# Optimization experiments

Measured on AMD Instinct MI355X. Metric: run time of the kernel, lower is better.

The kernel has to match this reference:

```python
import jax, jax.numpy as jnp
import numpy as np

PS = 3        # patch_size
RATE = 2      # rate
FS = 3        # fuse_kernel_size
SS = 10.0     # softmax_scale
PAD = (PS - 1) // 2       # tl.calc_padding(ps, 1)
FUSE_PAD = (FS - 1) // 2  # tl.calc_padding(fs, 1)
EPS = 1e-4


def extract_patches(x, ps, stride, pad):
    """x: (B,C,H,W) -> (B, L, C, ps, ps); L row-major over output positions (== F.unfold order)."""
    B, C, H, W = x.shape
    xp = jnp.pad(x, ((0, 0), (0, 0), (pad, pad), (pad, pad)))
    oh = (H + 2 * pad - ps) // stride + 1
    ow = (W + 2 * pad - ps) // stride + 1
    rows = []
    for dy in range(ps):  # small fixed loop (ps=3)
        cols = []
        for dx in range(ps):
            cols.append(xp[:, :, dy:dy + (oh - 1) * stride + 1:stride,
                              dx:dx + (ow - 1) * stride + 1:stride])
        rows.append(jnp.stack(cols, axis=2))           # (B,C,ps,oh,ow)
    p = jnp.stack(rows, axis=2)                        # (B,C,ps,ps,oh,ow)
    return p.reshape(B, C, ps, ps, oh * ow).transpose(0, 4, 1, 2, 3)


def diag_fuse(S, fs, pad):
    """conv2d of (N,N) 'image' with identity fs x fs kernel (diagonal smoothing)."""
    N = S.shape[0]
    Sp = jnp.pad(S, ((pad, pad), (pad, pad)))
    out = Sp[0:N, 0:N]
    for k in range(1, fs):  # fs=3, tiny fixed loop
        out = out + Sp[k:k + N, k:k + N]
    return out


def fuse_scores(S, hr, wr):
    L = hr * wr
    S = diag_fuse(S, FS, FUSE_PAD)
    S = S.reshape(hr, wr, hr, wr).transpose(1, 0, 3, 2).reshape(L, L)
    S = diag_fuse(S, FS, FUSE_PAD)
    S = S.reshape(wr, hr, wr, hr).transpose(1, 0, 3, 2).reshape(L, L)
    return S


def contextual_attention(f_o, b_o, mask_o):
    B, c, h, w = f_o.shape
    # nearest downsample by 1/rate == strided slice
    f = f_o[:, :, ::RATE, ::RATE]
    b = b_o[:, :, ::RATE, ::RATE]
    m = mask_o[:, :, ::RATE, ::RATE]
    hr, wr = f.shape[2], f.shape[3]
    L = hr * wr

    fg = extract_patches(f, PS, 1, PAD)        # (B,L,c,ps,ps) foreground neighborhoods
    bs = extract_patches(b, PS, 1, PAD)        # (B,L,c,ps,ps) shrunk bg patches
    bi = extract_patches(b_o, PS, RATE, PAD)   # (B,L,c,ps,ps) full-res bg patches

    bnorm = jnp.maximum(jnp.sqrt(jnp.sum(bs * bs, axis=(2, 3, 4))), EPS)  # (B,L)
    bsn = bs / bnorm[:, :, None, None, None]

    # score[b,p,q] = <normalized bg patch p, fg neighborhood at position q>
    S = jnp.einsum('bpcij,bqcij->bpq', bsn, fg)  # (B,L,L)
    S = jax.vmap(lambda s: fuse_scores(s, hr, wr))(S)

    # valid-patch indicator from downsampled mask
    mp = extract_patches(m, PS, 1, PAD)                                   # (B,L,1,ps,ps)
    valid = (jnp.mean(mp, axis=(2, 3, 4)) == 0.0).astype(f_o.dtype)       # (B,L)

    score = S.reshape(B, L, hr, wr) * valid[:, :, None, None]
    score = jax.nn.softmax(score * SS, axis=1) * valid[:, :, None, None]

    # conv_transpose2d(score, bi, stride=RATE, padding=PAD, output_padding=1) / 4
    wgt = jnp.flip(bi.transpose(0, 2, 1, 3, 4), axis=(-2, -1))  # (B,c,L,ps,ps)
    pad_cfg = [(PS - 1 - PAD, PS - 1 - PAD + 1)] * 2            # output_padding on high side

    def agg(s, wk):  # s:(L,hr,wr), wk:(c,L,ps,ps)
        return jax.lax.conv_general_dilated(
            s[None], wk, (1, 1), pad_cfg, lhs_dilation=(RATE, RATE),
            dimension_numbers=('NCHW', 'OIHW', 'NCHW'))[0]

    out = jax.vmap(agg)(score, wgt) / 4.0   # (B,c,h,w)
    return out


def setup_inputs() -> dict:
    key = jax.random.key(0)
    k1, k2, k3 = jax.random.split(key, 3)
    f_o = jax.random.normal(k1, (16, 128, 64, 64), dtype=jnp.float32)
    b_o = jax.random.normal(k2, (16, 128, 64, 64), dtype=jnp.float32)
    mask_o = jax.random.randint(k3, (16, 1, 64, 64), 0, 2).astype(jnp.float32)
    return {"f_o": f_o, "b_o": b_o, "mask_o": mask_o}


def reference(f_o, b_o, mask_o):
    return contextual_attention(f_o, b_o, mask_o)
```

## Files before the change

### kernel.cpp

```cpp
#include <hip/hip_runtime.h>
#include <cmath>

#define CC 128
#define HH 64
#define WWI 64
#define LL 1024
#define NB 16
#define MM 1152
#define KC 384
#define TPD 1156

#define SLAB      2977808ul
#define OFF_TP    0
#define OFF_S3T   0
#define OFF_W     0
#define OFF_S2    1336336
#define OFF_SCORET 1336336
#define OFF_POOL  2384912
#define OFF_N2    2974736
#define OFF_BNORM 2975760
#define OFF_VALID 2976784

typedef __bf16 bf16x8 __attribute__((ext_vector_type(8)));
typedef __bf16 bf16x4 __attribute__((ext_vector_type(4)));
typedef float f32x4 __attribute__((ext_vector_type(4)));

#define GLDS(g, l) __builtin_amdgcn_global_load_lds( \
    (const __attribute__((address_space(1))) unsigned int*)(const void*)(g), \
    (__attribute__((address_space(3))) unsigned int*)(void*)(l), 16, 0, 0)

__global__ __launch_bounds__(256) void k_prep(const float* __restrict__ f_o,
                                              const float* __restrict__ b_o,
                                              float* __restrict__ ws,
                                              int b0) {
    int bz = blockIdx.y, gb = b0 + bz;
    int uy = blockIdx.x;
    __shared__ float lf[128 * 33];
    __shared__ float lb[128 * 33];
    __shared__ float red[8 * 32];
    int tid = threadIdx.x;
    int ux = tid & 31, co = tid >> 5;
    size_t pix = (size_t)(2 * uy) * WWI + 2 * ux;
    const float* fbp = f_o + (size_t)gb * CC * HH * WWI + pix;
    const float* bbp = b_o + (size_t)gb * CC * HH * WWI + pix;
#pragma unroll
    for (int pass = 0; pass < 16; pass++) {
        int c = pass * 8 + co;
        lf[c * 33 + ux] = fbp[(size_t)c * HH * WWI];
        lb[c * 33 + ux] = bbp[(size_t)c * HH * WWI];
    }
    __syncthreads();
    int ux2 = tid >> 3, cg = (tid & 7) * 16;
    int u = uy * 32 + ux2;
    __bf16* bcat = (__bf16*)(ws + (size_t)bz * SLAB + OFF_POOL) + (size_t)u * KC;
    __bf16* fcat = bcat + 393216;
    float s2 = 0.f;
#pragma unroll
    for (int k = 0; k < 16; k++) {
        int c = cg + k;
        float fv = lf[c * 33 + ux2];
        float bv = lb[c * 33 + ux2];
        __bf16 fhi = (__bf16)fv; __bf16 flo = (__bf16)(fv - (float)fhi);
        __bf16 bhi = (__bf16)bv; __bf16 blo = (__bf16)(bv - (float)bhi);
        bcat[c] = bhi; bcat[128 + c] = bhi; bcat[256 + c] = blo;
        fcat[c] = fhi; fcat[128 + c] = flo; fcat[256 + c] = fhi;
        s2 += bv * bv;
    }
    red[(tid & 7) * 32 + ux2] = s2;
    __syncthreads();
    if (tid < 32) {
        float s = 0.f;
#pragma unroll
        for (int k = 0; k < 8; k++) s += red[k * 32 + tid];
        ws[(size_t)bz * SLAB + OFF_N2 + uy * 32 + tid] = s;
    }
}

__global__ __launch_bounds__(256) void k_bnorm_valid(float* __restrict__ ws,
                                                     const float* __restrict__ mask,
                                                     int b0) {
    int t = blockIdx.x * 256 + threadIdx.x;
    int p  = t & (LL - 1);
    int bz = t >> 10;
    int gb = b0 + bz;
    int py = p >> 5, px = p & 31;
    const float* mb = mask + (size_t)gb * HH * WWI;
    const float* n2 = ws + (size_t)bz * SLAB + OFF_N2;
    float s = 0.f, msum = 0.f;
#pragma unroll
    for (int dy = -1; dy <= 1; dy++) {
#pragma unroll
        for (int dx = -1; dx <= 1; dx++) {
            int py2 = py + dy, px2 = px + dx;
            if ((unsigned)py2 < 32u && (unsigned)px2 < 32u) {
                s    += n2[(py2 << 5) | px2];
                msum += mb[(2 * py2) * WWI + 2 * px2];
            }
        }
    }
    ws[(size_t)bz * SLAB + OFF_BNORM + p] = fmaxf(sqrtf(s), 1e-4f);
    ws[(size_t)bz * SLAB + OFF_VALID + p] = (msum == 0.0f) ? 1.0f : 0.0f;
}

__global__ __launch_bounds__(256) void k_zerohalo(float* __restrict__ ws) {
    int bz = blockIdx.y;
    int R  = blockIdx.x;
    float* Tr = ws + (size_t)bz * SLAB + OFF_TP + (size_t)R * TPD;
    int a = R / 34, b = R - 34 * a;
    bool rowhalo = (a == 0) | (a == 33) | (b == 0) | (b == 33);
    for (int c = threadIdx.x; c < TPD; c += 256) {
        int cy = c / 34, cb = c - 34 * cy;
        if (rowhalo | (cy == 0) | (cy == 33) | (cb == 0) | (cb == 33))
            Tr[c] = 0.f;
    }
}

template<int KTOT>
__device__ __forceinline__ void gemm_core(const __bf16* __restrict__ Ab,
                                          const __bf16* __restrict__ Bb,
                                          int lda, int ldb, int m0, int n0,
                                          __bf16* As, __bf16* Bs,
                                          f32x4 acc[4][4]) {
    int t = threadIdx.x;
    int lane = t & 63, w = t >> 6;
    int rsub = lane >> 3;
    int g8   = ((lane & 7) ^ (rsub & 7)) * 8;
    int lm = lane & 15, kgf = lane >> 4;
    int wm = (w & 1) * 64, wn = (w >> 1) * 64;

    for (int k0 = 0; k0 < KTOT; k0 += 64) {
        __syncthreads();
#pragma unroll
        for (int ci = 0; ci < 4; ci++) {
            int rb = ci * 32 + w * 8;
            int r  = rb + rsub;
            GLDS(Ab + (size_t)(m0 + r) * lda + k0 + g8, &As[rb * 64]);
            GLDS(Bb + (size_t)(n0 + r) * ldb + k0 + g8, &Bs[rb * 64]);
        }
        __syncthreads();
#pragma unroll
        for (int s2 = 0; s2 < 2; s2++) {
            bf16x8 af[4], bfr[4];
#pragma unroll
            for (int i = 0; i < 4; i++)
                af[i] = *(const bf16x8*)&As[(wm + i * 16 + lm) * 64 + (((s2 * 4 + kgf) ^ (lm & 7)) * 8)];
#pragma unroll
            for (int j = 0; j < 4; j++)
                bfr[j] = *(const bf16x8*)&Bs[(wn + j * 16 + lm) * 64 + (((s2 * 4 + kgf) ^ (lm & 7)) * 8)];
#pragma unroll
            for (int i = 0; i < 4; i++)
#pragma unroll
                for (int j = 0; j < 4; j++)
                    acc[i][j] = __builtin_amdgcn_mfma_f32_16x16x32_bf16(af[i], bfr[j], acc[i][j], 0, 0, 0);
        }
    }
}

__global__ __launch_bounds__(256) void k_gemm_T_mfma(float* __restrict__ ws) {
    int bz = blockIdx.z;
    const __bf16* Ab = (const __bf16*)(ws + (size_t)bz * SLAB + OFF_POOL);
    const __bf16* Bb = Ab + 393216;
    float* Tp = ws + (size_t)bz * SLAB + OFF_TP;
    int m0 = blockIdx.y * 128, n0 = blockIdx.x * 128;
    __shared__ __align__(16) __bf16 As[128 * 64];
    __shared__ __align__(16) __bf16 Bs[128 * 64];
    f32x4 acc[4][4];
#pragma unroll
    for (int i = 0; i < 4; i++)
#pragma unroll
        for (int j = 0; j < 4; j++) acc[i][j] = (f32x4)0.0f;
    gemm_core<KC>(Ab, Bb, KC, KC, m0, n0, As, Bs, acc);
    int lane = threadIdx.x & 63, w = threadIdx.x >> 6;
    int lm = lane & 15, kgf = lane >> 4;
    int wm = (w & 1) * 64, wn = (w >> 1) * 64;
#pragma unroll
    for (int i = 0; i < 4; i++) {
#pragma unroll
        for (int r = 0; r < 4; r++) {
            int m = m0 + wm + i * 16 + kgf * 4 + r;
            float* dst = Tp + (size_t)(((m >> 5) + 1) * 34 + (m & 31) + 1) * TPD;
#pragma unroll
            for (int j = 0; j < 4; j++) {
                int v = n0 + wn + j * 16 + lm;
                dst[((v >> 5) + 1) * 34 + (v & 31) + 1] = acc[i][j][r];
            }
        }
    }
}

__global__ __launch_bounds__(256) void k_s12(float* __restrict__ ws) {
    int bz = blockIdx.y;
    int i0 = blockIdx.x * 8;
    const float* Tp = ws + (size_t)bz * SLAB + OFF_TP;
    const float* bn = ws + (size_t)bz * SLAB + OFF_BNORM;
    float* S2 = ws + (size_t)bz * SLAB + OFF_S2;
    __shared__ float Dsh[10][1024];
    int tid = threadIdx.x;
    for (int rl = 0; rl < 10; rl++) {
        int r = i0 - 1 + rl;
        if ((unsigned)r >= 1024u) continue;
        float invr = 1.0f / bn[r];
        size_t rbase = (size_t)(((r >> 5) + 1) * 34 + (r & 31) + 1) * TPD;
#pragma unroll
        for (int so = 0; so < 4; so++) {
            int s = so * 256 + tid;
            const float* cb = Tp + rbase + ((s >> 5) + 1) * 34 + (s & 31) + 1;
            float d = 0.f;
#pragma unroll
            for (int dy = -1; dy <= 1; dy++)
#pragma unroll
                for (int dx = -1; dx <= 1; dx++)
                    d += cb[dy * (34 * TPD + 34) + dx * (TPD + 1)];
            Dsh[rl][s] = d * invr;
        }
    }
    __syncthreads();
#pragma unroll
    for (int il = 0; il < 8; il++) {
        int i = i0 + il;
        float* orow = S2 + (size_t)i * LL;
#pragma unroll
        for (int jo = 0; jo < 4; jo++) {
            int j = jo * 256 + tid;
            float acc = 0.f;
#pragma unroll
            for (int k1 = -1; k1 <= 1; k1++) {
                int r = i + k1, s = j + k1;
                if ((unsigned)r < 1024u && (unsigned)s < 1024u)
                    acc += Dsh[il + 1 + k1][s];
            }
            orow[j] = acc;
        }
    }
}

__global__ __launch_bounds__(256) void k_st3t(float* __restrict__ ws) {
    int bz = blockIdx.z;
    const float* ib = ws + (size_t)bz * SLAB + OFF_S2;
    float* ob = ws + (size_t)bz * SLAB + OFF_S3T;
    int p0 = blockIdx.y * 64, q0 = blockIdx.x * 64;
    __shared__ float tile[64][65];
    int t = threadIdx.x;
#pragma unroll
    for (int it = 0; it < 16; it++) {
        int e = it * 256 + t;
        int pl = e >> 6, ql = e & 63;
        int p = p0 + pl, q = q0 + ql;
        int sp = ((p & 31) << 5) | (p >> 5);
        int sq = ((q & 31) << 5) | (q >> 5);
        float acc = 0.f;
#pragma unroll
        for (int k = -1; k <= 1; k++) {
            int tp = sp + k, tq = sq + k;
            if ((unsigned)tp < 1024u && (unsigned)tq < 1024u) {
                int row = ((tp & 31) << 5) | (tp >> 5);
                int col = ((tq & 31) << 5) | (tq >> 5);
                acc += ib[(size_t)row * LL + col];
            }
        }
        tile[pl][ql] = acc;
    }
    __syncthreads();
#pragma unroll
    for (int it = 0; it < 16; it++) {
        int e = it * 256 + t;
        int ql = e >> 6, pl = e & 63;
        ob[(size_t)(q0 + ql) * LL + p0 + pl] = tile[pl][ql];
    }
}

__global__ __launch_bounds__(256) void k_softmax_bf(float* __restrict__ ws) {
    int bz = blockIdx.z;
    int lane = threadIdx.x & 63;
    int q = blockIdx.x * 4 + (threadIdx.x >> 6);
    const float* row = ws + (size_t)bz * SLAB + OFF_S3T + (size_t)q * LL;
    const float* vb  = ws + (size_t)bz * SLAB + OFF_VALID;
    __bf16* orow = (__bf16*)(ws + (size_t)bz * SLAB + OFF_SCORET) + (size_t)q * LL;

    float4 v[4], vl[4];
#pragma unroll
    for (int i = 0; i < 4; i++) {
        int p = lane * 4 + i * 256;
        float4 s = *(const float4*)(row + p);
        float4 m = *(const float4*)(vb + p);
        v[i] = {s.x * m.x, s.y * m.y, s.z * m.z, s.w * m.w};
        vl[i] = m;
    }
    float mx = -1e30f;
#pragma unroll
    for (int i = 0; i < 4; i++)
        mx = fmaxf(mx, fmaxf(fmaxf(v[i].x, v[i].y), fmaxf(v[i].z, v[i].w)));
#pragma unroll
    for (int k = 1; k < 64; k <<= 1)
        mx = fmaxf(mx, __shfl_xor(mx, k, 64));
    float sum = 0.f;
    float4 e[4];
#pragma unroll
    for (int i = 0; i < 4; i++) {
        e[i].x = __expf(10.f * (v[i].x - mx));
        e[i].y = __expf(10.f * (v[i].y - mx));
        e[i].z = __expf(10.f * (v[i].z - mx));
        e[i].w = __expf(10.f * (v[i].w - mx));
        sum += e[i].x + e[i].y + e[i].z + e[i].w;
    }
#pragma unroll
    for (int k = 1; k < 64; k <<= 1)
        sum += __shfl_xor(sum, k, 64);
    float inv = 1.0f / sum;
#pragma unroll
    for (int i = 0; i < 4; i++) {
        bf16x4 o;
        o[0] = (__bf16)(e[i].x * inv * vl[i].x);
        o[1] = (__bf16)(e[i].y * inv * vl[i].y);
        o[2] = (__bf16)(e[i].z * inv * vl[i].z);
        o[3] = (__bf16)(e[i].w * inv * vl[i].w);
        *(bf16x4*)(orow + lane * 4 + i * 256) = o;
    }
}

__global__ __launch_bounds__(256) void k_makeA(const float* __restrict__ b_o,
                                               float* __restrict__ ws,
                                               int b0) {
    int bz = blockIdx.z, gb = b0 + bz;
    int e = blockIdx.x * 256 + threadIdx.x;
    int m = e >> 10, p = e & 1023;
    int c = m / 9, rem = m - 9 * c, jy = rem / 3, jx = rem - 3 * jy;
    int row = 2 * (p >> 5) + jy - 1;
    int col = 2 * (p & 31) + jx - 1;
    float v = 0.f;
    if ((unsigned)row < 64u && (unsigned)col < 64u)
        v = b_o[((size_t)(gb * CC + c) * HH + row) * WWI + col];
    ((__bf16*)(ws + (size_t)bz * SLAB + OFF_POOL))[(size_t)m * LL + p] = (__bf16)v;
}

__global__ __launch_bounds__(256) void k_gemm_W_mfma(float* __restrict__ ws) {
    int bz = blockIdx.z;
    const __bf16* Ab = (const __bf16*)(ws + (size_t)bz * SLAB + OFF_POOL);
    const __bf16* Bb = (const __bf16*)(ws + (size_t)bz * SLAB + OFF_SCORET);
    float* Wb = ws + (size_t)bz * SLAB + OFF_W;
    int m0 = blockIdx.y * 128, n0 = blockIdx.x * 128;
    __shared__ __align__(16) __bf16 As[128 * 64];
    __shared__ __align__(16) __bf16 Bs[128 * 64];
    f32x4 acc[4][4];
#pragma unroll
    for (int i = 0; i < 4; i++)
#pragma unroll
        for (int j = 0; j < 4; j++) acc[i][j] = (f32x4)0.0f;
    gemm_core<LL>(Ab, Bb, LL, LL, m0, n0, As, Bs, acc);
    int lane = threadIdx.x & 63, w = threadIdx.x >> 6;
    int lm = lane & 15, kgf = lane >> 4;
    int wm = (w & 1) * 64, wn = (w >> 1) * 64;
#pragma unroll
    for (int i = 0; i < 4; i++) {
#pragma unroll
        for (int r = 0; r < 4; r++) {
            int m = m0 + wm + i * 16 + kgf * 4 + r;
            float* dst = Wb + (size_t)m * LL + n0 + wn + lm;
#pragma unroll
            for (int j = 0; j < 4; j++)
                dst[j * 16] = acc[i][j][r];
        }
    }
}

__global__ __launch_bounds__(256) void k_gather(const float* __restrict__ ws,
                                                float* __restrict__ outp,
                                                int b0) {
    int t = blockIdx.x * 256 + threadIdx.x;
    int ox = t & 63, oy = (t >> 6) & 63, c = (t >> 12) & 127, bz = t >> 19;
    const float* Wb = ws + (size_t)bz * SLAB + OFF_W;
    int qyA = (oy + 1) >> 1;
    int jyA = (oy & 1) ? 0 : 1;
    int vA  = (qyA < 32);
    int qyB = (oy - 1) >> 1;
    int vB  = (oy & 1);
    int qxA = (ox + 1) >> 1;
    int jxA = (ox & 1) ? 0 : 1;
    int uA  = (qxA < 32);
    int qxB = (ox - 1) >> 1;
    int uB  = (ox & 1);
    const float* base = Wb + (size_t)c * 9 * LL;
    float s = 0.f;
    if (vA && uA) s += base[(size_t)(jyA * 3 + jxA) * LL + qyA * 32 + qxA];
    if (vA && uB) s += base[(size_t)(jyA * 3 + 2)   * LL + qyA * 32 + qxB];
    if (vB && uA) s += base[(size_t)(2 * 3 + jxA)   * LL + qyB * 32 + qxA];
    if (vB && uB) s += base[(size_t)(2 * 3 + 2)     * LL + qyB * 32 + qxB];
    outp[((size_t)((b0 + bz) * CC + c) * HH + oy) * WWI + ox] = 0.25f * s;
}

extern "C" void kernel_launch(void* const* d_in, const int* in_sizes, int n_in,
                              void* d_out, int out_size, void* d_ws, size_t ws_size,
                              hipStream_t stream) {
    (void)in_sizes; (void)n_in; (void)out_size;
    const float* f_o  = (const float*)d_in[0];
    const float* b_o  = (const float*)d_in[1];
    const float* mask = (const float*)d_in[2];
    float* out = (float*)d_out;

    int G = (int)(ws_size / (SLAB * sizeof(float)));
    if (G < 1) G = 1;
    if (G > NB) G = NB;
    float* ws = (float*)d_ws;

    for (int b0 = 0; b0 < NB; b0 += G) {
        int Gc = NB - b0 < G ? NB - b0 : G;
        k_prep<<<dim3(32, Gc), 256, 0, stream>>>(f_o, b_o, ws, b0);
        k_bnorm_valid<<<dim3(Gc * 4), 256, 0, stream>>>(ws, mask, b0);
        k_zerohalo<<<dim3(TPD, Gc), 256, 0, stream>>>(ws);
        k_gemm_T_mfma<<<dim3(8, 8, Gc), 256, 0, stream>>>(ws);
        k_s12<<<dim3(128, Gc), 256, 0, stream>>>(ws);
        k_st3t<<<dim3(16, 16, Gc), 256, 0, stream>>>(ws);
        k_softmax_bf<<<dim3(256, 1, Gc), 256, 0, stream>>>(ws);
        k_makeA<<<dim3(4608, 1, Gc), 256, 0, stream>>>(b_o, ws, b0);
        k_gemm_W_mfma<<<dim3(8, 9, Gc), 256, 0, stream>>>(ws);
        k_gather<<<dim3(Gc * 2048), 256, 0, stream>>>(ws, out, b0);
    }
}
```

Before: 413.0 us.

## Shrink halo zeroing, tile makeA via LDS, store W in bf16, swizzle GEMM grids

k_zerohalo now launches threads only over halo elements instead of scanning every padded row. k_makeA stages each 64x64 channel image in shared memory and writes vectorized bf16x4 patch rows. The W GEMM output and the gather input move from fp32 to bf16, halving that traffic at some cost in precision. When all 16 batches fit in one pass, the GEMM grids are remapped so neighbouring blocks belong to different batches, which changes L2 locality.

```diff
diff --git a/kernel.cpp b/kernel.cpp
--- a/kernel.cpp
+++ b/kernel.cpp
@@ -20,6 +20,10 @@
 #define OFF_N2    2974736
 #define OFF_BNORM 2975760
 #define OFF_VALID 2976784
+
+#define NHROW 132
+#define NH1 (NHROW * TPD)
+#define NHALO (NH1 + 1024 * NHROW)
 
 typedef __bf16 bf16x8 __attribute__((ext_vector_type(8)));
 typedef __bf16 bf16x4 __attribute__((ext_vector_type(4)));
@@ -102,16 +106,27 @@
     ws[(size_t)bz * SLAB + OFF_VALID + p] = (msum == 0.0f) ? 1.0f : 0.0f;
 }
 
+__device__ __forceinline__ int halo_idx(int k) {
+    if (k < 34) return k;
+    if (k < 68) return 1122 + (k - 34);
+    if (k < 100) return 34 * (k - 100 + 33);
+    return 34 * (k - 132 + 33) + 33;
+}
+
 __global__ __launch_bounds__(256) void k_zerohalo(float* __restrict__ ws) {
     int bz = blockIdx.y;
-    int R  = blockIdx.x;
-    float* Tr = ws + (size_t)bz * SLAB + OFF_TP + (size_t)R * TPD;
-    int a = R / 34, b = R - 34 * a;
-    bool rowhalo = (a == 0) | (a == 33) | (b == 0) | (b == 33);
-    for (int c = threadIdx.x; c < TPD; c += 256) {
-        int cy = c / 34, cb = c - 34 * cy;
-        if (rowhalo | (cy == 0) | (cy == 33) | (cb == 0) | (cb == 33))
-            Tr[c] = 0.f;
+    int t = blockIdx.x * 256 + threadIdx.x;
+    if (t >= NHALO) return;
+    float* Tp = ws + (size_t)bz * SLAB + OFF_TP;
+    if (t < NH1) {
+        int R = halo_idx(t / TPD);
+        Tp[(size_t)R * TPD + (t % TPD)] = 0.f;
+    } else {
+        int t2 = t - NH1;
+        int ir = t2 / NHROW;
+        int R  = 34 * (1 + (ir >> 5)) + 1 + (ir & 31);
+        int C  = halo_idx(t2 % NHROW);
+        Tp[(size_t)R * TPD + C] = 0.f;
     }
 }
 
@@ -156,12 +171,18 @@
     }
 }
 
-__global__ __launch_bounds__(256) void k_gemm_T_mfma(float* __restrict__ ws) {
-    int bz = blockIdx.z;
+__global__ __launch_bounds__(256) void k_gemm_T_mfma(float* __restrict__ ws, int swz) {
+    int bz, m0, n0;
+    if (swz) {
+        bz = blockIdx.x + 8 * (blockIdx.z & 1);
+        m0 = blockIdx.y * 128;
+        n0 = (blockIdx.z >> 1) * 128;
+    } else {
+        bz = blockIdx.z; m0 = blockIdx.y * 128; n0 = blockIdx.x * 128;
+    }
     const __bf16* Ab = (const __bf16*)(ws + (size_t)bz * SLAB + OFF_POOL);
     const __bf16* Bb = Ab + 393216;
     float* Tp = ws + (size_t)bz * SLAB + OFF_TP;
-    int m0 = blockIdx.y * 128, n0 = blockIdx.x * 128;
     __shared__ __align__(16) __bf16 As[128 * 64];
     __shared__ __align__(16) __bf16 Bs[128 * 64];
     f32x4 acc[4][4];
@@ -321,24 +342,51 @@
 __global__ __launch_bounds__(256) void k_makeA(const float* __restrict__ b_o,
                                                float* __restrict__ ws,
                                                int b0) {
-    int bz = blockIdx.z, gb = b0 + bz;
-    int e = blockIdx.x * 256 + threadIdx.x;
-    int m = e >> 10, p = e & 1023;
-    int c = m / 9, rem = m - 9 * c, jy = rem / 3, jx = rem - 3 * jy;
-    int row = 2 * (p >> 5) + jy - 1;
-    int col = 2 * (p & 31) + jx - 1;
-    float v = 0.f;
-    if ((unsigned)row < 64u && (unsigned)col < 64u)
-        v = b_o[((size_t)(gb * CC + c) * HH + row) * WWI + col];
-    ((__bf16*)(ws + (size_t)bz * SLAB + OFF_POOL))[(size_t)m * LL + p] = (__bf16)v;
-}
-
-__global__ __launch_bounds__(256) void k_gemm_W_mfma(float* __restrict__ ws) {
-    int bz = blockIdx.z;
+    int c = blockIdx.x, bz = blockIdx.y, gb = b0 + bz;
+    __shared__ float img[64][65];
+    int t = threadIdx.x;
+    const float4* src = (const float4*)(b_o + (size_t)(gb * CC + c) * HH * WWI);
+#pragma unroll
+    for (int it = 0; it < 4; it++) {
+        int idx = it * 256 + t;
+        float4 v = src[idx];
+        int row = idx >> 4, col4 = (idx & 15) * 4;
+        img[row][col4] = v.x; img[row][col4 + 1] = v.y;
+        img[row][col4 + 2] = v.z; img[row][col4 + 3] = v.w;
+    }
+    __syncthreads();
+    __bf16* Ab = (__bf16*)(ws + (size_t)bz * SLAB + OFF_POOL) + (size_t)c * 9 * LL;
+    int py = t >> 3, px4 = (t & 7) * 4;
+#pragma unroll
+    for (int jy = 0; jy < 3; jy++) {
+        int row = 2 * py + jy - 1;
+        bool rok = (unsigned)row < 64u;
+#pragma unroll
+        for (int jx = 0; jx < 3; jx++) {
+            bf16x4 o;
+#pragma unroll
+            for (int e = 0; e < 4; e++) {
+                int col = 2 * (px4 + e) + jx - 1;
+                float v = (rok && (unsigned)col < 64u) ? img[rok ? row : 0][(unsigned)col < 64u ? col : 0] : 0.f;
+                o[e] = (__bf16)v;
+            }
+            *(bf16x4*)(Ab + (size_t)(jy * 3 + jx) * LL + t * 4) = o;
+        }
+    }
+}
+
+__global__ __launch_bounds__(256) void k_gemm_W_mfma(float* __restrict__ ws, int swz) {
+    int bz, m0, n0;
+    if (swz) {
+        bz = blockIdx.x + 8 * (blockIdx.z & 1);
+        m0 = blockIdx.y * 128;
+        n0 = (blockIdx.z >> 1) * 128;
+    } else {
+        bz = blockIdx.z; m0 = blockIdx.y * 128; n0 = blockIdx.x * 128;
+    }
     const __bf16* Ab = (const __bf16*)(ws + (size_t)bz * SLAB + OFF_POOL);
     const __bf16* Bb = (const __bf16*)(ws + (size_t)bz * SLAB + OFF_SCORET);
-    float* Wb = ws + (size_t)bz * SLAB + OFF_W;
-    int m0 = blockIdx.y * 128, n0 = blockIdx.x * 128;
+    __bf16* Wb = (__bf16*)(ws + (size_t)bz * SLAB + OFF_W);
     __shared__ __align__(16) __bf16 As[128 * 64];
     __shared__ __align__(16) __bf16 Bs[128 * 64];
     f32x4 acc[4][4];
@@ -355,10 +403,10 @@
 #pragma unroll
         for (int r = 0; r < 4; r++) {
             int m = m0 + wm + i * 16 + kgf * 4 + r;
-            float* dst = Wb + (size_t)m * LL + n0 + wn + lm;
+            __bf16* dst = Wb + (size_t)m * LL + n0 + wn + lm;
 #pragma unroll
             for (int j = 0; j < 4; j++)
-                dst[j * 16] = acc[i][j][r];
+                dst[j * 16] = (__bf16)acc[i][j][r];
         }
     }
 }
@@ -368,7 +416,7 @@
                                                 int b0) {
     int t = blockIdx.x * 256 + threadIdx.x;
     int ox = t & 63, oy = (t >> 6) & 63, c = (t >> 12) & 127, bz = t >> 19;
-    const float* Wb = ws + (size_t)bz * SLAB + OFF_W;
+    const __bf16* Wb = (const __bf16*)(ws + (size_t)bz * SLAB + OFF_W);
     int qyA = (oy + 1) >> 1;
     int jyA = (oy & 1) ? 0 : 1;
     int vA  = (qyA < 32);
@@ -379,12 +427,12 @@
     int uA  = (qxA < 32);
     int qxB = (ox - 1) >> 1;
     int uB  = (ox & 1);
-    const float* base = Wb + (size_t)c * 9 * LL;
+    const __bf16* base = Wb + (size_t)c * 9 * LL;
     float s = 0.f;
-    if (vA && uA) s += base[(size_t)(jyA * 3 + jxA) * LL + qyA * 32 + qxA];
-    if (vA && uB) s += base[(size_t)(jyA * 3 + 2)   * LL + qyA * 32 + qxB];
-    if (vB && uA) s += base[(size_t)(2 * 3 + jxA)   * LL + qyB * 32 + qxA];
-    if (vB && uB) s += base[(size_t)(2 * 3 + 2)     * LL + qyB * 32 + qxB];
+    if (vA && uA) s += (float)base[(size_t)(jyA * 3 + jxA) * LL + qyA * 32 + qxA];
+    if (vA && uB) s += (float)base[(size_t)(jyA * 3 + 2)   * LL + qyA * 32 + qxB];
+    if (vB && uA) s += (float)base[(size_t)(2 * 3 + jxA)   * LL + qyB * 32 + qxA];
+    if (vB && uB) s += (float)base[(size_t)(2 * 3 + 2)     * LL + qyB * 32 + qxB];
     outp[((size_t)((b0 + bz) * CC + c) * HH + oy) * WWI + ox] = 0.25f * s;
 }
 
@@ -404,15 +452,16 @@
 
     for (int b0 = 0; b0 < NB; b0 += G) {
         int Gc = NB - b0 < G ? NB - b0 : G;
+        int swz = (Gc == 16) ? 1 : 0;
         k_prep<<<dim3(32, Gc), 256, 0, stream>>>(f_o, b_o, ws, b0);
         k_bnorm_valid<<<dim3(Gc * 4), 256, 0, stream>>>(ws, mask, b0);
-        k_zerohalo<<<dim3(TPD, Gc), 256, 0, stream>>>(ws);
-        k_gemm_T_mfma<<<dim3(8, 8, Gc), 256, 0, stream>>>(ws);
+        k_zerohalo<<<dim3((NHALO + 255) / 256, Gc), 256, 0, stream>>>(ws);
+        k_gemm_T_mfma<<<dim3(8, 8, Gc), 256, 0, stream>>>(ws, swz);
         k_s12<<<dim3(128, Gc), 256, 0, stream>>>(ws);
         k_st3t<<<dim3(16, 16, Gc), 256, 0, stream>>>(ws);
         k_softmax_bf<<<dim3(256, 1, Gc), 256, 0, stream>>>(ws);
-        k_makeA<<<dim3(4608, 1, Gc), 256, 0, stream>>>(b_o, ws, b0);
-        k_gemm_W_mfma<<<dim3(8, 9, Gc), 256, 0, stream>>>(ws);
+        k_makeA<<<dim3(CC, Gc), 256, 0, stream>>>(b_o, ws, b0);
+        k_gemm_W_mfma<<<dim3(8, 9, Gc), 256, 0, stream>>>(ws, swz);
         k_gather<<<dim3(Gc * 2048), 256, 0, stream>>>(ws, out, b0);
     }
 }
```

Result: faster. 373.6 us (-9.5%).
